# Optimization experiments

Measured on AMD Instinct MI355X. Metric: run time of the kernel, lower is better.

## Reference

```python
import jax, jax.numpy as jnp
import numpy as np

NV, NSEG, SEGSZ, GRID = 778, 16, 49, 32
SCALE_FACTOR = 0.1


def grid_sample_3d(vol, pts):
    """Trilinear grid_sample, align_corners=True, zeros padding.
    vol: [D,H,W]; pts: [N,3] with (x,y,z) in [-1,1] (x indexes W, z indexes D).
    """
    D, H, W = vol.shape
    fx = (pts[:, 0] + 1.0) * 0.5 * (W - 1)
    fy = (pts[:, 1] + 1.0) * 0.5 * (H - 1)
    fz = (pts[:, 2] + 1.0) * 0.5 * (D - 1)
    x0f, y0f, z0f = jnp.floor(fx), jnp.floor(fy), jnp.floor(fz)
    wx, wy, wz = fx - x0f, fy - y0f, fz - z0f
    x0 = x0f.astype(jnp.int32)
    y0 = y0f.astype(jnp.int32)
    z0 = z0f.astype(jnp.int32)
    out = jnp.zeros(pts.shape[0], vol.dtype)
    for dz in (0, 1):
        zz = z0 + dz
        ww_z = wz if dz else (1.0 - wz)
        for dy in (0, 1):
            yy = y0 + dy
            ww_zy = ww_z * (wy if dy else (1.0 - wy))
            for dx in (0, 1):
                xx = x0 + dx
                w = ww_zy * (wx if dx else (1.0 - wx))
                valid = (xx >= 0) & (xx < W) & (yy >= 0) & (yy < H) & (zz >= 0) & (zz < D)
                v = vol[jnp.clip(zz, 0, D - 1), jnp.clip(yy, 0, H - 1), jnp.clip(xx, 0, W - 1)]
                out = out + jnp.where(valid, v, 0.0) * w
    return out


def _boxes(segv):
    # segv: [B,16,S,3] -> center [B,16,3], scale [B,16]  (no_grad in original)
    mn = segv.min(axis=2)
    mx = segv.max(axis=2)
    center = 0.5 * (mn + mx)                       # mean of (min, max)
    scale = (1.0 + SCALE_FACTOR) * 0.5 * (mx - mn).max(axis=-1)
    return jax.lax.stop_gradient(center), jax.lax.stop_gradient(scale)


def _cross_sample(seg_src, center, scale, phi, seg):
    # seg_src [B,I,S,3]; center [B,J,3]; scale [B,J]; phi [J,B,G,G,G]
    B = seg_src.shape[0]
    coords = (seg_src[:, :, None, :, :] - center[:, None, :, None, :]) / scale[:, None, :, None, None]
    pts = coords.transpose(2, 0, 1, 3, 4).reshape(NSEG, B, NSEG * SEGSZ, 3)  # [J,B,M,3]
    vals = jax.vmap(jax.vmap(grid_sample_3d))(phi, pts)                      # [J,B,M]
    vals = vals.reshape(NSEG, B, NSEG, SEGSZ).transpose(1, 2, 0, 3)          # [B,I,J,S]
    phisum = vals.sum(axis=2)                                                # [B,I,S]
    orisum = (vals * scale[:, None, :, None]).sum(axis=2)                    # [B,I,S]
    flat = seg.reshape(-1)
    out = jnp.zeros((B, NV), jnp.float32).at[:, flat].add(phisum.reshape(B, -1))
    ori = jnp.zeros((B, NV), jnp.float32).at[:, flat].add(orisum.reshape(B, -1))
    return out, ori


def setup_inputs() -> dict:
    key = jax.random.key(0)
    k1, k2, k3, k4 = jax.random.split(key, 4)
    bs = 128
    vertices = jax.random.normal(k1, (bs, 2, NV, 3), dtype=jnp.float32)
    seg = jax.random.randint(k2, (NSEG, SEGSZ), 0, NV).astype(jnp.int32)
    phi_right = jax.random.uniform(k3, (NSEG, bs, GRID, GRID, GRID), dtype=jnp.float32)
    phi_left = jax.random.uniform(k4, (NSEG, bs, GRID, GRID, GRID), dtype=jnp.float32)
    return {"vertices": vertices, "phi_right": phi_right, "phi_left": phi_left, "seg": seg}


def reference(vertices, phi_right, phi_left, seg):
    left_vert = vertices[:, 1]   # [B,778,3]
    right_vert = vertices[:, 0]
    segL = left_vert[:, seg]     # [B,16,S,3]
    segR = right_vert[:, seg]
    cL, sL = _boxes(segL)
    cR, sR = _boxes(segR)
    out_left, _ = _cross_sample(segL, cR, sR, phi_right, seg)
    out_right, _ = _cross_sample(segR, cL, sL, phi_left, seg)
    num_hand = 2
    loss = (out_left / num_hand ** 2 + out_right / num_hand ** 2).sum(axis=1)  # [B]
    return loss
```

## Files before the change

### kernel.cpp

```cpp
#include <hip/hip_runtime.h>

#define NVV   778
#define NSEG  16
#define SEGSZ 49
#define GRIDN 32
#define BATCH 128
#define NPTS  784
#define VOLSZ (GRIDN * GRIDN * GRIDN)
#define NBLK  512
#define VPB   8
#define PFLT  8192

typedef float f4v __attribute__((ext_vector_type(4)));
#define NTLD(p) __builtin_nontemporal_load((const f4v*)(p))

#define STAGE(DST, SRC) { \
    const float* s_ = (SRC) + (wv << 11) + (lane << 2); \
    float*       d_ = (DST) + (wv << 11) + (lane << 2); \
    f4v c0 = NTLD(s_ + 0 * 256); \
    f4v c1 = NTLD(s_ + 1 * 256); \
    f4v c2 = NTLD(s_ + 2 * 256); \
    f4v c3 = NTLD(s_ + 3 * 256); \
    f4v c4 = NTLD(s_ + 4 * 256); \
    f4v c5 = NTLD(s_ + 5 * 256); \
    f4v c6 = NTLD(s_ + 6 * 256); \
    f4v c7 = NTLD(s_ + 7 * 256); \
    *(f4v*)(d_ + 0 * 256) = c0; \
    *(f4v*)(d_ + 1 * 256) = c1; \
    *(f4v*)(d_ + 2 * 256) = c2; \
    *(f4v*)(d_ + 3 * 256) = c3; \
    *(f4v*)(d_ + 4 * 256) = c4; \
    *(f4v*)(d_ + 5 * 256) = c5; \
    *(f4v*)(d_ + 6 * 256) = c6; \
    *(f4v*)(d_ + 7 * 256) = c7; }

__device__ __forceinline__ float tapxy(const float* slab, int x0, int y0,
                                       float wx, float wy)
{
    float s = 0.f;
    #pragma unroll
    for (int dy = 0; dy < 2; ++dy) {
        int yy = y0 + dy;
        if (yy < 0 || yy >= GRIDN) continue;
        float wyv = dy ? wy : 1.f - wy;
        const float* row = slab + yy * GRIDN;
        #pragma unroll
        for (int dx = 0; dx < 2; ++dx) {
            int xx = x0 + dx;
            if (xx < 0 || xx >= GRIDN) continue;
            s += wyv * (dx ? wx : 1.f - wx) * row[xx];
        }
    }
    return s;
}

#define TAP1(Q, BASE, J) \
    if (a##J) { \
        if (z##J >= 0 && (z##J >> 3) == (Q)) \
            acc##J += (1.f - w##J##z) * tapxy((BASE) + (z##J - 8 * (Q)) * 1024, x##J, y##J, w##J##x, w##J##y); \
        if ((z##J + 1) <= 31 && ((z##J + 1) >> 3) == (Q)) \
            acc##J += w##J##z * tapxy((BASE) + (z##J + 1 - 8 * (Q)) * 1024, x##J, y##J, w##J##x, w##J##y); \
    }
#define TAPALL(Q, BASE) \
    TAP1(Q, BASE, 1) TAP1(Q, BASE, 2) TAP1(Q, BASE, 3) \
    if (has4) { TAP1(Q, BASE, 4) }

#define SETUP(J, PX, PY, PZ) { \
    float fx = ((PX) - b4.x) * b4.w * 15.5f + 15.5f; \
    float fy = ((PY) - b4.y) * b4.w * 15.5f + 15.5f; \
    float fz = ((PZ) - b4.z) * b4.w * 15.5f + 15.5f; \
    a##J = (fx > -1.f && fx < 32.f && fy > -1.f && fy < 32.f && \
            fz > -1.f && fz < 32.f); \
    float xf = floorf(fx), yf = floorf(fy), zf = floorf(fz); \
    w##J##x = fx - xf; w##J##y = fy - yf; w##J##z = fz - zf; \
    x##J = (int)xf; y##J = (int)yf; z##J = (int)zf; acc##J = 0.f; }

__global__ __launch_bounds__(512, 4) void sample_kernel(
    const float* __restrict__ vertices, const int* __restrict__ seg,
    const float* __restrict__ phiR, const float* __restrict__ phiL,
    float* __restrict__ loss)
{
    __shared__ __align__(16) float P0[PFLT];
    __shared__ __align__(16) float P1[PFLT];
    __shared__ float4 sbox[VPB];
    __shared__ float wsum[4];

    const int tid  = threadIdx.x;
    const int bx   = blockIdx.x;
    const int k    = bx & (NSEG - 1);
    const int wv   = tid >> 6;
    const int lane = tid & 63;
    const bool producer = (wv < 4);
    const int ct   = tid - 256;

    auto phiPtr = [&](int it) {
        int vid  = bx + NBLK * it;
        int b    = (vid >> 4) & (BATCH - 1);
        int pass = vid >> 11;
        return (pass == 0 ? phiR : phiL) + ((size_t)k * BATCH + b) * VOLSZ;
    };
    auto vertBase = [&](int it) {
        int vid  = bx + NBLK * it;
        int b    = (vid >> 4) & (BATCH - 1);
        int srcS = (vid >> 11) == 0 ? 1 : 0;
        return vertices + ((size_t)b * 2 + srcS) * NVV * 3;
    };
    auto bOf = [&](int it) { return ((bx + NBLK * it) >> 4) & (BATCH - 1); };

    int pvi1 = 0, pvi2 = 0, pvi3 = 0, pvi4 = 0;
    bool has4 = false;
    if (!producer) {
        pvi1 = seg[ct];
        pvi2 = seg[ct + 256];
        pvi3 = seg[ct + 512];
        has4 = (ct + 768) < NPTS;
        pvi4 = has4 ? seg[ct + 768] : 0;
    }

    {
        int vidw    = bx + NBLK * wv;
        int bbw     = (vidw >> 4) & (BATCH - 1);
        int boxSide = ((vidw >> 11) == 0) ? 0 : 1;
        bool bact   = lane < SEGSZ;
        int bvi     = bact ? seg[k * SEGSZ + lane] : 0;
        const float* bvp = vertices + (((size_t)bbw * 2 + boxSide) * NVV + bvi) * 3;
        float x = bvp[0], y = bvp[1], z = bvp[2];
        float mnx = bact ? x : 1e30f, mxx = bact ? x : -1e30f;
        float mny = bact ? y : 1e30f, mxy = bact ? y : -1e30f;
        float mnz = bact ? z : 1e30f, mxz = bact ? z : -1e30f;
        #pragma unroll
        for (int m = 32; m; m >>= 1) {
            mnx = fminf(mnx, __shfl_xor(mnx, m));
            mxx = fmaxf(mxx, __shfl_xor(mxx, m));
            mny = fminf(mny, __shfl_xor(mny, m));
            mxy = fmaxf(mxy, __shfl_xor(mxy, m));
            mnz = fminf(mnz, __shfl_xor(mnz, m));
            mxz = fmaxf(mxz, __shfl_xor(mxz, m));
        }
        if (lane == 0) {
            float ext = fmaxf(fmaxf(mxx - mnx, mxy - mny), mxz - mnz);
            sbox[wv] = make_float4(0.5f * (mnx + mxx), 0.5f * (mny + mxy),
                                   0.5f * (mnz + mxz), 1.0f / (0.55f * ext));
        }
    }

    float p1x = 0.f, p1y = 0.f, p1z = 0.f, p2x = 0.f, p2y = 0.f, p2z = 0.f;
    float p3x = 0.f, p3y = 0.f, p3z = 0.f, p4x = 0.f, p4y = 0.f, p4z = 0.f;
    if (producer) {
        STAGE(P0, phiPtr(0))
    } else {
        const float* vb = vertBase(0);
        p1x = vb[pvi1 * 3]; p1y = vb[pvi1 * 3 + 1]; p1z = vb[pvi1 * 3 + 2];
        p2x = vb[pvi2 * 3]; p2y = vb[pvi2 * 3 + 1]; p2z = vb[pvi2 * 3 + 2];
        p3x = vb[pvi3 * 3]; p3y = vb[pvi3 * 3 + 1]; p3z = vb[pvi3 * 3 + 2];
        if (has4) {
            p4x = vb[pvi4 * 3]; p4y = vb[pvi4 * 3 + 1]; p4z = vb[pvi4 * 3 + 2];
        }
    }
    __syncthreads();

    float n1x = 0.f, n1y = 0.f, n1z = 0.f, n2x = 0.f, n2y = 0.f, n2z = 0.f;
    float n3x = 0.f, n3y = 0.f, n3z = 0.f, n4x = 0.f, n4y = 0.f, n4z = 0.f;

    for (int v = 0; v < VPB; ++v) {
        const bool more = (v + 1 < VPB);
        bool a1 = false, a2 = false, a3 = false, a4 = false;
        int x1, y1, z1, x2, y2, z2, x3, y3, z3, x4, y4, z4;
        float w1x, w1y, w1z, w2x, w2y, w2z, w3x, w3y, w3z, w4x, w4y, w4z;
        float acc1 = 0.f, acc2 = 0.f, acc3 = 0.f, acc4 = 0.f;

        if (producer) {
            STAGE(P1, phiPtr(v) + PFLT)
        } else {
            if (v > 0 && ct == 0) {
                float tot = wsum[0] + wsum[1] + wsum[2] + wsum[3];
                atomicAdd(loss + bOf(v - 1), tot * 0.25f);
            }
            float4 b4 = sbox[v];
            SETUP(1, p1x, p1y, p1z)
            SETUP(2, p2x, p2y, p2z)
            SETUP(3, p3x, p3y, p3z)
            if (has4) { SETUP(4, p4x, p4y, p4z) }
            TAPALL(0, P0)
        }
        __syncthreads();

        if (producer) {
            STAGE(P0, phiPtr(v) + 2 * PFLT)
        } else {
            TAPALL(1, P1)
        }
        __syncthreads();

        if (producer) {
            STAGE(P1, phiPtr(v) + 3 * PFLT)
        } else {
            TAPALL(2, P0)
            if (more) {
                const float* vb = vertBase(v + 1);
                n1x = vb[pvi1 * 3]; n1y = vb[pvi1 * 3 + 1]; n1z = vb[pvi1 * 3 + 2];
                n2x = vb[pvi2 * 3]; n2y = vb[pvi2 * 3 + 1]; n2z = vb[pvi2 * 3 + 2];
                n3x = vb[pvi3 * 3]; n3y = vb[pvi3 * 3 + 1]; n3z = vb[pvi3 * 3 + 2];
                if (has4) {
                    n4x = vb[pvi4 * 3]; n4y = vb[pvi4 * 3 + 1]; n4z = vb[pvi4 * 3 + 2];
                }
            }
        }
        __syncthreads();

        if (producer) {
            if (more) { STAGE(P0, phiPtr(v + 1)) }
        } else {
            TAPALL(3, P1)
            float acc = acc1 + acc2 + acc3 + acc4;
            #pragma unroll
            for (int off = 32; off; off >>= 1)
                acc += __shfl_down(acc, off);
            if (lane == 0) wsum[wv - 4] = acc;
        }
        __syncthreads();

        p1x = n1x; p1y = n1y; p1z = n1z; p2x = n2x; p2y = n2y; p2z = n2z;
        p3x = n3x; p3y = n3y; p3z = n3z; p4x = n4x; p4y = n4y; p4z = n4z;
    }

    if (!producer && ct == 0) {
        float tot = wsum[0] + wsum[1] + wsum[2] + wsum[3];
        atomicAdd(loss + bOf(VPB - 1), tot * 0.25f);
    }
}

extern "C" void kernel_launch(void* const* d_in, const int* in_sizes, int n_in,
                              void* d_out, int out_size, void* d_ws, size_t ws_size,
                              hipStream_t stream) {
    const float* vertices = (const float*)d_in[0];
    const float* phiR     = (const float*)d_in[1];
    const float* phiL     = (const float*)d_in[2];
    const int*   seg      = (const int*)d_in[3];
    float* loss = (float*)d_out;

    hipMemsetAsync(d_out, 0, (size_t)out_size * sizeof(float), stream);

    sample_kernel<<<NBLK, 512, 0, stream>>>(vertices, seg, phiR, phiL, loss);
}
```

Baseline: 101.4 us.

## Halve staging chunks, double blocks, rebalance producer/consumer waves

Stage each volume in eight 4-slice chunks of 16KB instead of four 8-slice chunks of 32KB. The grid doubles to 1024 blocks, each handling 4 volumes instead of 8. Producer waves drop from 4 to 2 and consumer waves rise from 4 to 6, so each consumer thread now handles up to 3 points instead of 4. The smaller LDS footprint and the higher launch-bounds occupancy target aim to fit more blocks per CU and hide load latency better, at the cost of twice as many block barriers per volume and possible register pressure.

Result: slower. 168.9 us (+66.5%).

```diff
diff --git a/kernel.cpp b/kernel.cpp
--- a/kernel.cpp
+++ b/kernel.cpp
@@ -7,9 +7,9 @@
 #define BATCH 128
 #define NPTS  784
 #define VOLSZ (GRIDN * GRIDN * GRIDN)
-#define NBLK  512
-#define VPB   8
-#define PFLT  8192
+#define NBLK  1024
+#define VPB   4
+#define PFLT  4096
 
 typedef float f4v __attribute__((ext_vector_type(4)));
 #define NTLD(p) __builtin_nontemporal_load((const f4v*)(p))
@@ -56,14 +56,14 @@
 
 #define TAP1(Q, BASE, J) \
     if (a##J) { \
-        if (z##J >= 0 && (z##J >> 3) == (Q)) \
-            acc##J += (1.f - w##J##z) * tapxy((BASE) + (z##J - 8 * (Q)) * 1024, x##J, y##J, w##J##x, w##J##y); \
-        if ((z##J + 1) <= 31 && ((z##J + 1) >> 3) == (Q)) \
-            acc##J += w##J##z * tapxy((BASE) + (z##J + 1 - 8 * (Q)) * 1024, x##J, y##J, w##J##x, w##J##y); \
+        if (z##J >= 0 && (z##J >> 2) == (Q)) \
+            acc##J += (1.f - w##J##z) * tapxy((BASE) + (z##J - 4 * (Q)) * 1024, x##J, y##J, w##J##x, w##J##y); \
+        if ((z##J + 1) <= 31 && ((z##J + 1) >> 2) == (Q)) \
+            acc##J += w##J##z * tapxy((BASE) + (z##J + 1 - 4 * (Q)) * 1024, x##J, y##J, w##J##x, w##J##y); \
     }
 #define TAPALL(Q, BASE) \
-    TAP1(Q, BASE, 1) TAP1(Q, BASE, 2) TAP1(Q, BASE, 3) \
-    if (has4) { TAP1(Q, BASE, 4) }
+    TAP1(Q, BASE, 1) TAP1(Q, BASE, 2) \
+    if (has3) { TAP1(Q, BASE, 3) }
 
 #define SETUP(J, PX, PY, PZ) { \
     float fx = ((PX) - b4.x) * b4.w * 15.5f + 15.5f; \
@@ -75,7 +75,7 @@
     w##J##x = fx - xf; w##J##y = fy - yf; w##J##z = fz - zf; \
     x##J = (int)xf; y##J = (int)yf; z##J = (int)zf; acc##J = 0.f; }
 
-__global__ __launch_bounds__(512, 4) void sample_kernel(
+__global__ __launch_bounds__(512, 8) void sample_kernel(
     const float* __restrict__ vertices, const int* __restrict__ seg,
     const float* __restrict__ phiR, const float* __restrict__ phiL,
     float* __restrict__ loss)
@@ -83,15 +83,15 @@
     __shared__ __align__(16) float P0[PFLT];
     __shared__ __align__(16) float P1[PFLT];
     __shared__ float4 sbox[VPB];
-    __shared__ float wsum[4];
+    __shared__ float wsum[6];
 
     const int tid  = threadIdx.x;
     const int bx   = blockIdx.x;
     const int k    = bx & (NSEG - 1);
     const int wv   = tid >> 6;
     const int lane = tid & 63;
-    const bool producer = (wv < 4);
-    const int ct   = tid - 256;
+    const bool producer = (wv < 2);
+    const int ct   = tid - 128;
 
     auto phiPtr = [&](int it) {
         int vid  = bx + NBLK * it;
@@ -107,17 +107,16 @@
     };
     auto bOf = [&](int it) { return ((bx + NBLK * it) >> 4) & (BATCH - 1); };
 
-    int pvi1 = 0, pvi2 = 0, pvi3 = 0, pvi4 = 0;
-    bool has4 = false;
+    int pvi1 = 0, pvi2 = 0, pvi3 = 0;
+    bool has3 = false;
     if (!producer) {
         pvi1 = seg[ct];
-        pvi2 = seg[ct + 256];
-        pvi3 = seg[ct + 512];
-        has4 = (ct + 768) < NPTS;
-        pvi4 = has4 ? seg[ct + 768] : 0;
-    }
-
-    {
+        pvi2 = seg[ct + 384];
+        has3 = (ct + 768) < NPTS;
+        pvi3 = has3 ? seg[ct + 768] : 0;
+    }
+
+    if (wv < VPB) {
         int vidw    = bx + NBLK * wv;
         int bbw     = (vidw >> 4) & (BATCH - 1);
         int boxSide = ((vidw >> 11) == 0) ? 0 : 1;
@@ -145,87 +144,78 @@
     }
 
     float p1x = 0.f, p1y = 0.f, p1z = 0.f, p2x = 0.f, p2y = 0.f, p2z = 0.f;
-    float p3x = 0.f, p3y = 0.f, p3z = 0.f, p4x = 0.f, p4y = 0.f, p4z = 0.f;
+    float p3x = 0.f, p3y = 0.f, p3z = 0.f;
     if (producer) {
         STAGE(P0, phiPtr(0))
     } else {
         const float* vb = vertBase(0);
         p1x = vb[pvi1 * 3]; p1y = vb[pvi1 * 3 + 1]; p1z = vb[pvi1 * 3 + 2];
         p2x = vb[pvi2 * 3]; p2y = vb[pvi2 * 3 + 1]; p2z = vb[pvi2 * 3 + 2];
-        p3x = vb[pvi3 * 3]; p3y = vb[pvi3 * 3 + 1]; p3z = vb[pvi3 * 3 + 2];
-        if (has4) {
-            p4x = vb[pvi4 * 3]; p4y = vb[pvi4 * 3 + 1]; p4z = vb[pvi4 * 3 + 2];
+        if (has3) {
+            p3x = vb[pvi3 * 3]; p3y = vb[pvi3 * 3 + 1]; p3z = vb[pvi3 * 3 + 2];
         }
     }
     __syncthreads();
 
     float n1x = 0.f, n1y = 0.f, n1z = 0.f, n2x = 0.f, n2y = 0.f, n2z = 0.f;
-    float n3x = 0.f, n3y = 0.f, n3z = 0.f, n4x = 0.f, n4y = 0.f, n4z = 0.f;
+    float n3x = 0.f, n3y = 0.f, n3z = 0.f;
 
     for (int v = 0; v < VPB; ++v) {
         const bool more = (v + 1 < VPB);
-        bool a1 = false, a2 = false, a3 = false, a4 = false;
-        int x1, y1, z1, x2, y2, z2, x3, y3, z3, x4, y4, z4;
-        float w1x, w1y, w1z, w2x, w2y, w2z, w3x, w3y, w3z, w4x, w4y, w4z;
-        float acc1 = 0.f, acc2 = 0.f, acc3 = 0.f, acc4 = 0.f;
-
-        if (producer) {
-            STAGE(P1, phiPtr(v) + PFLT)
-        } else {
-            if (v > 0 && ct == 0) {
-                float tot = wsum[0] + wsum[1] + wsum[2] + wsum[3];
-                atomicAdd(loss + bOf(v - 1), tot * 0.25f);
+        bool a1 = false, a2 = false, a3 = false;
+        int x1, y1, z1, x2, y2, z2, x3, y3, z3;
+        float w1x, w1y, w1z, w2x, w2y, w2z, w3x, w3y, w3z;
+        float acc1 = 0.f, acc2 = 0.f, acc3 = 0.f;
+
+        #pragma unroll
+        for (int q = 0; q < 8; ++q) {
+            const float* tapbuf = (q & 1) ? P1 : P0;
+            float*       stgbuf = (q & 1) ? P0 : P1;
+
+            if (producer) {
+                if (q < 7) {
+                    STAGE(stgbuf, phiPtr(v) + (q + 1) * PFLT)
+                } else if (more) {
+                    STAGE(stgbuf, phiPtr(v + 1))
+                }
+            } else {
+                if (q == 0) {
+                    if (v > 0 && ct == 0) {
+                        float tot = wsum[0] + wsum[1] + wsum[2] +
+                                    wsum[3] + wsum[4] + wsum[5];
+                        atomicAdd(loss + bOf(v - 1), tot * 0.25f);
+                    }
+                    float4 b4 = sbox[v];
+                    SETUP(1, p1x, p1y, p1z)
+                    SETUP(2, p2x, p2y, p2z)
+                    if (has3) { SETUP(3, p3x, p3y, p3z) }
+                }
+                TAPALL(q, tapbuf)
+                if (q == 6 && more) {
+                    const float* vb = vertBase(v + 1);
+                    n1x = vb[pvi1 * 3]; n1y = vb[pvi1 * 3 + 1]; n1z = vb[pvi1 * 3 + 2];
+                    n2x = vb[pvi2 * 3]; n2y = vb[pvi2 * 3 + 1]; n2z = vb[pvi2 * 3 + 2];
+                    if (has3) {
+                        n3x = vb[pvi3 * 3]; n3y = vb[pvi3 * 3 + 1]; n3z = vb[pvi3 * 3 + 2];
+                    }
+                }
+                if (q == 7) {
+                    float acc = acc1 + acc2 + acc3;
+                    #pragma unroll
+                    for (int off = 32; off; off >>= 1)
+                        acc += __shfl_down(acc, off);
+                    if (lane == 0) wsum[wv - 2] = acc;
+                }
             }
-            float4 b4 = sbox[v];
-            SETUP(1, p1x, p1y, p1z)
-            SETUP(2, p2x, p2y, p2z)
-            SETUP(3, p3x, p3y, p3z)
-            if (has4) { SETUP(4, p4x, p4y, p4z) }
-            TAPALL(0, P0)
-        }
-        __syncthreads();
-
-        if (producer) {
-            STAGE(P0, phiPtr(v) + 2 * PFLT)
-        } else {
-            TAPALL(1, P1)
-        }
-        __syncthreads();
-
-        if (producer) {
-            STAGE(P1, phiPtr(v) + 3 * PFLT)
-        } else {
-            TAPALL(2, P0)
-            if (more) {
-                const float* vb = vertBase(v + 1);
-                n1x = vb[pvi1 * 3]; n1y = vb[pvi1 * 3 + 1]; n1z = vb[pvi1 * 3 + 2];
-                n2x = vb[pvi2 * 3]; n2y = vb[pvi2 * 3 + 1]; n2z = vb[pvi2 * 3 + 2];
-                n3x = vb[pvi3 * 3]; n3y = vb[pvi3 * 3 + 1]; n3z = vb[pvi3 * 3 + 2];
-                if (has4) {
-                    n4x = vb[pvi4 * 3]; n4y = vb[pvi4 * 3 + 1]; n4z = vb[pvi4 * 3 + 2];
-                }
-            }
-        }
-        __syncthreads();
-
-        if (producer) {
-            if (more) { STAGE(P0, phiPtr(v + 1)) }
-        } else {
-            TAPALL(3, P1)
-            float acc = acc1 + acc2 + acc3 + acc4;
-            #pragma unroll
-            for (int off = 32; off; off >>= 1)
-                acc += __shfl_down(acc, off);
-            if (lane == 0) wsum[wv - 4] = acc;
-        }
-        __syncthreads();
+            __syncthreads();
+        }
 
         p1x = n1x; p1y = n1y; p1z = n1z; p2x = n2x; p2y = n2y; p2z = n2z;
-        p3x = n3x; p3y = n3y; p3z = n3z; p4x = n4x; p4y = n4y; p4z = n4z;
+        p3x = n3x; p3y = n3y; p3z = n3z;
     }
 
     if (!producer && ct == 0) {
-        float tot = wsum[0] + wsum[1] + wsum[2] + wsum[3];
+        float tot = wsum[0] + wsum[1] + wsum[2] + wsum[3] + wsum[4] + wsum[5];
         atomicAdd(loss + bOf(VPB - 1), tot * 0.25f);
     }
 }
```
